# Kernel optimization log

Measured on AMD Instinct MI355X. Metric: run time of the kernel, lower is better.

The kernel has to match this reference:

```python
import jax, jax.numpy as jnp
import numpy as np

B, N, D = 1, 65536, 1024
H = 512
R = 16  # num_regions
C = 2   # num_classes

def _gelu(x):
    return jax.nn.gelu(x, approximate=False)  # torch nn.GELU default is exact erf

def setup_inputs() -> dict:
    key = jax.random.key(0)
    ks = jax.random.split(key, 16)
    s = 0.02
    return {
        "embeddings": jax.random.normal(ks[0], (B, N, D), dtype=jnp.float32),
        # region_encoder: Linear(D,H) + GELU (dropout=0 in eval)
        "W1": jax.random.normal(ks[1], (D, H), dtype=jnp.float32) * s,
        "b1": jnp.zeros((H,), dtype=jnp.float32),
        # region_attention: Linear(H,H//2) -> tanh -> Linear(H//2,1)
        "Wa1": jax.random.normal(ks[2], (H, H // 2), dtype=jnp.float32) * s,
        "ba1": jnp.zeros((H // 2,), dtype=jnp.float32),
        "Wa2": jax.random.normal(ks[3], (H // 2, 1), dtype=jnp.float32) * s,
        "ba2": jnp.zeros((1,), dtype=jnp.float32),
        # slide_encoder: Linear(H,H) + GELU
        "Ws": jax.random.normal(ks[4], (H, H), dtype=jnp.float32) * s,
        "bs": jnp.zeros((H,), dtype=jnp.float32),
        # slide_attention
        "Wsa1": jax.random.normal(ks[5], (H, H // 2), dtype=jnp.float32) * s,
        "bsa1": jnp.zeros((H // 2,), dtype=jnp.float32),
        "Wsa2": jax.random.normal(ks[6], (H // 2, 1), dtype=jnp.float32) * s,
        "bsa2": jnp.zeros((1,), dtype=jnp.float32),
        # classifier: Linear(H,H//2) -> GELU -> Linear(H//2,C)
        "Wc1": jax.random.normal(ks[7], (H, H // 2), dtype=jnp.float32) * s,
        "bc1": jnp.zeros((H // 2,), dtype=jnp.float32),
        "Wc2": jax.random.normal(ks[8], (H // 2, C), dtype=jnp.float32) * s,
        "bc2": jnp.zeros((C,), dtype=jnp.float32),
    }

def reference(embeddings, W1, b1, Wa1, ba1, Wa2, ba2, Ws, bs, Wsa1, bsa1, Wsa2, bsa2, Wc1, bc1, Wc2, bc2):
    b, n, d = embeddings.shape
    m = n // R  # patches per region
    # coords=None path: region_ids[i] = i % R, so region r holds indices r, r+R, ...
    # Equivalent regrouping via reshape+transpose: (B, M, R, D) -> (B, R, M, D)
    x = embeddings.reshape(b, m, R, d).transpose(0, 2, 1, 3)
    # region encoder
    region_emb = _gelu(jnp.einsum('brmd,dh->brmh', x, W1) + b1)  # (B,R,M,H)
    # region attention pooling
    scores = jnp.einsum('brmk,ko->brmo', jnp.tanh(jnp.einsum('brmh,hk->brmk', region_emb, Wa1) + ba1), Wa2) + ba2  # (B,R,M,1)
    attn = jax.nn.softmax(scores, axis=2)
    region_features = jnp.sum(region_emb * attn, axis=2)  # (B,R,H)
    # slide encoder + attention pooling over regions
    slide_emb = _gelu(jnp.einsum('brh,hg->brg', region_features, Ws) + bs)  # (B,R,H)
    sattn = jnp.einsum('brk,ko->bro', jnp.tanh(jnp.einsum('brh,hk->brk', slide_emb, Wsa1) + bsa1), Wsa2) + bsa2  # (B,R,1)
    sweights = jax.nn.softmax(sattn, axis=1)
    slide_rep = jnp.sum(slide_emb * sweights, axis=1)  # (B,H)
    # classifier
    logits = _gelu(slide_rep @ Wc1 + bc1) @ Wc2 + bc2  # (B,C)
    return logits
```

## Files before the change

### kernel.cpp

```cpp
#include <hip/hip_runtime.h>

#define NTOK 65536
#define DIN  1024
#define H    512
#define HH   256
#define NREG 16
#define MPR  4096

__device__ __forceinline__ unsigned short f2bf(float f) {
  unsigned u = __float_as_uint(f);
  u += 0x7fffu + ((u >> 16) & 1u);
  return (unsigned short)(u >> 16);
}
__device__ __forceinline__ float bf2f(unsigned short s) {
  return __uint_as_float(((unsigned)s) << 16);
}
__device__ __forceinline__ float gelu_exact(float x) {
  return 0.5f * x * (1.0f + erff(x * 0.70710678118654752440f));
}

typedef __attribute__((ext_vector_type(8))) short shortx8;
typedef __attribute__((ext_vector_type(4))) float floatx4;

__device__ __forceinline__ void gl_lds16(const void* g, void* l) {
  __builtin_amdgcn_global_load_lds(
      (const __attribute__((address_space(1))) void*)g,
      (__attribute__((address_space(3))) void*)l, 16, 0, 0);
}

__global__ __launch_bounds__(256) void k0_prep(const float* __restrict__ W1,
                                               const float* __restrict__ Wa1,
                                               unsigned short* __restrict__ W1t,
                                               unsigned short* __restrict__ Wa1t) {
  int idx = blockIdx.x * 256 + threadIdx.x;
  if (idx < DIN * H) {
    int n = idx >> 10, k = idx & 1023;
    W1t[idx] = f2bf(W1[k * H + n]);
  } else {
    int i2 = idx - DIN * H;
    int n = i2 >> 9, k = i2 & 511;
    Wa1t[i2] = f2bf(Wa1[k * HH + n]);
  }
}

__global__ __launch_bounds__(256) void k1_gemm1(const float* __restrict__ X,
                                                const unsigned short* __restrict__ W1t,
                                                const float* __restrict__ b1,
                                                unsigned short* __restrict__ Eb) {
  __shared__ __align__(16) short lA[128 * 32];
  __shared__ __align__(16) short lB[128 * 32];
  const int tid = threadIdx.x;
  const int colBase = blockIdx.x * 128;
  const int rowBase = blockIdx.y * 128;
  const int lane = tid & 63;
  const int wave = tid >> 6;
  const int wr = wave >> 1, wc = wave & 1;
  const int l15 = lane & 15, quad = lane >> 4;

  floatx4 acc[4][4] = {};

  for (int kb = 0; kb < DIN; kb += 32) {
    __syncthreads();
#pragma unroll
    for (int s = 0; s < 2; s++) {
      int c = tid + s * 256;
      gl_lds16(W1t + (size_t)(colBase + (c >> 2)) * DIN + kb + (c & 3) * 8, &lB[c * 8]);
    }
#pragma unroll
    for (int s = 0; s < 2; s++) {
      int c = tid + s * 256;
      const floatx4* src =
          (const floatx4*)(X + (size_t)(rowBase + (c >> 2)) * DIN + kb + (c & 3) * 8);
      floatx4 f0 = src[0], f1 = src[1];
      shortx8 h;
      h[0] = (short)f2bf(f0[0]); h[1] = (short)f2bf(f0[1]);
      h[2] = (short)f2bf(f0[2]); h[3] = (short)f2bf(f0[3]);
      h[4] = (short)f2bf(f1[0]); h[5] = (short)f2bf(f1[1]);
      h[6] = (short)f2bf(f1[2]); h[7] = (short)f2bf(f1[3]);
      *(shortx8*)(&lA[c * 8]) = h;
    }
    __syncthreads();
    shortx8 aF[4], bF[4];
#pragma unroll
    for (int i = 0; i < 4; i++)
      aF[i] = *(const shortx8*)(&lA[(wr * 64 + i * 16 + l15) * 32 + quad * 8]);
#pragma unroll
    for (int j = 0; j < 4; j++)
      bF[j] = *(const shortx8*)(&lB[(wc * 64 + j * 16 + l15) * 32 + quad * 8]);
#pragma unroll
    for (int i = 0; i < 4; i++)
#pragma unroll
      for (int j = 0; j < 4; j++)
        acc[i][j] = __builtin_amdgcn_mfma_f32_16x16x32_bf16(aF[i], bF[j], acc[i][j], 0, 0, 0);
  }

  const int row0 = rowBase + wr * 64;
  const int col0 = colBase + wc * 64;
#pragma unroll
  for (int j = 0; j < 4; j++) {
    int col = col0 + j * 16 + l15;
    float bias = b1[col];
#pragma unroll
    for (int i = 0; i < 4; i++) {
      int rb = row0 + i * 16 + quad * 4;
#pragma unroll
      for (int v = 0; v < 4; v++) {
        float x = acc[i][j][v] + bias;
        Eb[(size_t)(rb + v) * H + col] = f2bf(gelu_exact(x));
      }
    }
  }
}

__global__ __launch_bounds__(256) void k2_gemm2(const unsigned short* __restrict__ Eb,
                                                const unsigned short* __restrict__ Wa1t,
                                                const float* __restrict__ ba1,
                                                const float* __restrict__ Wa2,
                                                float* __restrict__ scores) {
  __shared__ __align__(16) short lA[128 * 32];
  __shared__ __align__(16) short lB[128 * 32];
  const int tid = threadIdx.x;
  const int colBase = blockIdx.x * 128;
  const int rowBase = blockIdx.y * 128;
  const int lane = tid & 63;
  const int wave = tid >> 6;
  const int wr = wave >> 1, wc = wave & 1;
  const int l15 = lane & 15, quad = lane >> 4;

  floatx4 acc[4][4] = {};

  for (int kb = 0; kb < H; kb += 32) {
    __syncthreads();
#pragma unroll
    for (int s = 0; s < 2; s++) {
      int c = tid + s * 256;
      gl_lds16(Eb + (size_t)(rowBase + (c >> 2)) * H + kb + (c & 3) * 8, &lA[c * 8]);
      gl_lds16(Wa1t + (size_t)(colBase + (c >> 2)) * H + kb + (c & 3) * 8, &lB[c * 8]);
    }
    __syncthreads();
    shortx8 aF[4], bF[4];
#pragma unroll
    for (int i = 0; i < 4; i++)
      aF[i] = *(const shortx8*)(&lA[(wr * 64 + i * 16 + l15) * 32 + quad * 8]);
#pragma unroll
    for (int j = 0; j < 4; j++)
      bF[j] = *(const shortx8*)(&lB[(wc * 64 + j * 16 + l15) * 32 + quad * 8]);
#pragma unroll
    for (int i = 0; i < 4; i++)
#pragma unroll
      for (int j = 0; j < 4; j++)
        acc[i][j] = __builtin_amdgcn_mfma_f32_16x16x32_bf16(aF[i], bF[j], acc[i][j], 0, 0, 0);
  }

  float p[4][4];
#pragma unroll
  for (int i = 0; i < 4; i++)
#pragma unroll
    for (int v = 0; v < 4; v++) p[i][v] = 0.0f;
#pragma unroll
  for (int j = 0; j < 4; j++) {
    int col = colBase + wc * 64 + j * 16 + l15;
    float bias = ba1[col];
    float wa2 = Wa2[col];
#pragma unroll
    for (int i = 0; i < 4; i++)
#pragma unroll
      for (int v = 0; v < 4; v++)
        p[i][v] += tanhf(acc[i][j][v] + bias) * wa2;
  }
#pragma unroll
  for (int i = 0; i < 4; i++)
#pragma unroll
    for (int v = 0; v < 4; v++) {
      float t = p[i][v];
      t += __shfl_xor(t, 1, 16);
      t += __shfl_xor(t, 2, 16);
      t += __shfl_xor(t, 4, 16);
      t += __shfl_xor(t, 8, 16);
      p[i][v] = t;
    }
  if (l15 == 0) {
    int row0 = rowBase + wr * 64 + quad * 4;
#pragma unroll
    for (int i = 0; i < 4; i++)
#pragma unroll
      for (int v = 0; v < 4; v++)
        atomicAdd(&scores[row0 + i * 16 + v], p[i][v]);
  }
}

__global__ __launch_bounds__(256) void k3a_softmax(const float* __restrict__ scores,
                                                   float* __restrict__ wts) {
  const int r = blockIdx.x, tid = threadIdx.x;
  __shared__ float red[256];
  float m = -1e30f;
  for (int j = tid; j < MPR; j += 256) m = fmaxf(m, scores[r + NREG * j]);
  red[tid] = m;
  __syncthreads();
  for (int s = 128; s > 0; s >>= 1) {
    if (tid < s) red[tid] = fmaxf(red[tid], red[tid + s]);
    __syncthreads();
  }
  float mx = red[0];
  __syncthreads();
  float sum = 0.0f;
  for (int j = tid; j < MPR; j += 256) sum += expf(scores[r + NREG * j] - mx);
  red[tid] = sum;
  __syncthreads();
  for (int s = 128; s > 0; s >>= 1) {
    if (tid < s) red[tid] += red[tid + s];
    __syncthreads();
  }
  float inv = 1.0f / red[0];
  for (int j = tid; j < MPR; j += 256)
    wts[r + NREG * j] = expf(scores[r + NREG * j] - mx) * inv;
}

__global__ __launch_bounds__(256) void k3b_wsum(const unsigned short* __restrict__ Eb,
                                                const float* __restrict__ wts,
                                                float* __restrict__ rf) {
  const int r = blockIdx.y;
  const int mc = blockIdx.x;
  const int tid = threadIdx.x;
  float a0 = 0.0f, a1 = 0.0f;
  for (int j = mc * 128; j < mc * 128 + 128; j++) {
    int n = r + NREG * j;
    float w = wts[n];
    unsigned v = *(const unsigned*)(Eb + (size_t)n * H + tid * 2);
    a0 += w * bf2f((unsigned short)(v & 0xffffu));
    a1 += w * bf2f((unsigned short)(v >> 16));
  }
  atomicAdd(&rf[r * H + tid * 2], a0);
  atomicAdd(&rf[r * H + tid * 2 + 1], a1);
}

__global__ __launch_bounds__(256) void k4a_slide(const float* __restrict__ rf,
                                                 const float* __restrict__ Ws,
                                                 const float* __restrict__ bs,
                                                 float* __restrict__ se) {
  const int r = blockIdx.x, tid = threadIdx.x;
  __shared__ float lrf[H];
  lrf[tid] = rf[r * H + tid];
  lrf[tid + 256] = rf[r * H + tid + 256];
  __syncthreads();
  float a0 = 0.0f, a1 = 0.0f;
  for (int k = 0; k < H; k++) {
    float x = lrf[k];
    a0 += x * Ws[k * H + tid];
    a1 += x * Ws[k * H + tid + 256];
  }
  se[r * H + tid] = gelu_exact(a0 + bs[tid]);
  se[r * H + tid + 256] = gelu_exact(a1 + bs[tid + 256]);
}

__global__ __launch_bounds__(256) void k4b_sscore(const float* __restrict__ se,
                                                  const float* __restrict__ Wsa1,
                                                  const float* __restrict__ bsa1,
                                                  const float* __restrict__ Wsa2,
                                                  const float* __restrict__ bsa2,
                                                  float* __restrict__ ss) {
  const int r = blockIdx.x, tid = threadIdx.x;
  __shared__ float lse[H];
  __shared__ float red[256];
  lse[tid] = se[r * H + tid];
  lse[tid + 256] = se[r * H + tid + 256];
  __syncthreads();
  float a = 0.0f;
  for (int k = 0; k < H; k++) a += lse[k] * Wsa1[k * HH + tid];
  red[tid] = tanhf(a + bsa1[tid]) * Wsa2[tid];
  __syncthreads();
  for (int s = 128; s > 0; s >>= 1) {
    if (tid < s) red[tid] += red[tid + s];
    __syncthreads();
  }
  if (tid == 0) ss[r] = red[0] + bsa2[0];
}

__global__ __launch_bounds__(256) void k4c_final(const float* __restrict__ se,
                                                 const float* __restrict__ ss,
                                                 const float* __restrict__ Wc1,
                                                 const float* __restrict__ bc1,
                                                 const float* __restrict__ Wc2,
                                                 const float* __restrict__ bc2,
                                                 float* __restrict__ out) {
  const int tid = threadIdx.x;
  __shared__ float srep[H];
  __shared__ float r0[256], r1[256];
  float mx = -1e30f;
  for (int i = 0; i < NREG; i++) mx = fmaxf(mx, ss[i]);
  float wv[NREG];
  float den = 0.0f;
  for (int i = 0; i < NREG; i++) { wv[i] = expf(ss[i] - mx); den += wv[i]; }
  float inv = 1.0f / den;
  float s0 = 0.0f, s1 = 0.0f;
  for (int i = 0; i < NREG; i++) {
    float w = wv[i] * inv;
    s0 += w * se[i * H + tid];
    s1 += w * se[i * H + tid + 256];
  }
  srep[tid] = s0;
  srep[tid + 256] = s1;
  __syncthreads();
  float a = 0.0f;
  for (int k = 0; k < H; k++) a += srep[k] * Wc1[k * HH + tid];
  float g = gelu_exact(a + bc1[tid]);
  r0[tid] = g * Wc2[tid * 2];
  r1[tid] = g * Wc2[tid * 2 + 1];
  __syncthreads();
  for (int s = 128; s > 0; s >>= 1) {
    if (tid < s) { r0[tid] += r0[tid + s]; r1[tid] += r1[tid + s]; }
    __syncthreads();
  }
  if (tid == 0) {
    out[0] = r0[0] + bc2[0];
    out[1] = r1[0] + bc2[1];
  }
}

extern "C" void kernel_launch(void* const* d_in, const int* in_sizes, int n_in,
                              void* d_out, int out_size, void* d_ws, size_t ws_size,
                              hipStream_t stream) {
  const float* X    = (const float*)d_in[0];
  const float* W1   = (const float*)d_in[1];
  const float* b1   = (const float*)d_in[2];
  const float* Wa1  = (const float*)d_in[3];
  const float* ba1  = (const float*)d_in[4];
  const float* Wa2  = (const float*)d_in[5];
  const float* Ws   = (const float*)d_in[7];
  const float* bs   = (const float*)d_in[8];
  const float* Wsa1 = (const float*)d_in[9];
  const float* bsa1 = (const float*)d_in[10];
  const float* Wsa2 = (const float*)d_in[11];
  const float* bsa2 = (const float*)d_in[12];
  const float* Wc1  = (const float*)d_in[13];
  const float* bc1  = (const float*)d_in[14];
  const float* Wc2  = (const float*)d_in[15];
  const float* bc2  = (const float*)d_in[16];
  float* out = (float*)d_out;

  char* ws = (char*)d_ws;
  constexpr size_t OFF_W1T  = 0;
  constexpr size_t OFF_WA1T = OFF_W1T + (size_t)H * DIN * 2;
  constexpr size_t OFF_EB   = OFF_WA1T + (size_t)HH * H * 2;
  constexpr size_t OFF_SC   = OFF_EB + (size_t)NTOK * H * 2;
  constexpr size_t OFF_RF   = OFF_SC + (size_t)NTOK * 4;
  constexpr size_t OFF_WT   = OFF_RF + (size_t)NREG * H * 4;
  constexpr size_t OFF_SE   = OFF_WT + (size_t)NTOK * 4;
  constexpr size_t OFF_SS   = OFF_SE + (size_t)NREG * H * 4;

  unsigned short* W1t  = (unsigned short*)(ws + OFF_W1T);
  unsigned short* Wa1t = (unsigned short*)(ws + OFF_WA1T);
  unsigned short* Eb   = (unsigned short*)(ws + OFF_EB);
  float* scores = (float*)(ws + OFF_SC);
  float* rf     = (float*)(ws + OFF_RF);
  float* wts    = (float*)(ws + OFF_WT);
  float* se     = (float*)(ws + OFF_SE);
  float* ssb    = (float*)(ws + OFF_SS);

  hipMemsetAsync(scores, 0, (size_t)NTOK * 4 + (size_t)NREG * H * 4, stream);

  k0_prep<<<(DIN * H + HH * H) / 256, 256, 0, stream>>>(W1, Wa1, W1t, Wa1t);
  k1_gemm1<<<dim3(4, 512), 256, 0, stream>>>(X, W1t, b1, Eb);
  k2_gemm2<<<dim3(2, 512), 256, 0, stream>>>(Eb, Wa1t, ba1, Wa2, scores);
  k3a_softmax<<<NREG, 256, 0, stream>>>(scores, wts);
  k3b_wsum<<<dim3(32, NREG), 256, 0, stream>>>(Eb, wts, rf);
  k4a_slide<<<NREG, 256, 0, stream>>>(rf, Ws, bs, se);
  k4b_sscore<<<NREG, 256, 0, stream>>>(se, Wsa1, bsa1, Wsa2, bsa2, ssb);
  k4c_final<<<1, 256, 0, stream>>>(se, ssb, Wc1, bc1, Wc2, bc2, out);
}
```

Before: 653.0 us.

## Pre-convert X to bf16 and swizzle LDS tiles in both GEMMs

Adds a separate kernel that converts the fp32 embeddings to bf16 once. GEMM1 can then load its A tile straight from global memory into LDS with direct loads instead of converting in registers each time. Both GEMMs get an XOR swizzle on the k-group layout in LDS to reduce bank conflicts on fragment reads. The trade-off is an extra full pass over X and a large bf16 workspace buffer.

```diff
diff --git a/kernel.cpp b/kernel.cpp
--- a/kernel.cpp
+++ b/kernel.cpp
@@ -26,6 +26,19 @@
   __builtin_amdgcn_global_load_lds(
       (const __attribute__((address_space(1))) void*)g,
       (__attribute__((address_space(3))) void*)l, 16, 0, 0);
+}
+
+__global__ __launch_bounds__(256) void kc_convert(const float* __restrict__ X,
+                                                  unsigned short* __restrict__ Xb) {
+  size_t i = ((size_t)blockIdx.x * 256 + threadIdx.x) * 8;
+  const floatx4* src = (const floatx4*)(X + i);
+  floatx4 f0 = src[0], f1 = src[1];
+  shortx8 h;
+  h[0] = (short)f2bf(f0[0]); h[1] = (short)f2bf(f0[1]);
+  h[2] = (short)f2bf(f0[2]); h[3] = (short)f2bf(f0[3]);
+  h[4] = (short)f2bf(f1[0]); h[5] = (short)f2bf(f1[1]);
+  h[6] = (short)f2bf(f1[2]); h[7] = (short)f2bf(f1[3]);
+  *(shortx8*)(Xb + i) = h;
 }
 
 __global__ __launch_bounds__(256) void k0_prep(const float* __restrict__ W1,
@@ -43,7 +56,8 @@
   }
 }
 
-__global__ __launch_bounds__(256) void k1_gemm1(const float* __restrict__ X,
+
+__global__ __launch_bounds__(256) void k1_gemm1(const unsigned short* __restrict__ Xb,
                                                 const unsigned short* __restrict__ W1t,
                                                 const float* __restrict__ b1,
                                                 unsigned short* __restrict__ Eb) {
@@ -56,6 +70,7 @@
   const int wave = tid >> 6;
   const int wr = wave >> 1, wc = wave & 1;
   const int l15 = lane & 15, quad = lane >> 4;
+  const int sw = (l15 >> 1) & 3;
 
   floatx4 acc[4][4] = {};
 
@@ -64,29 +79,19 @@
 #pragma unroll
     for (int s = 0; s < 2; s++) {
       int c = tid + s * 256;
-      gl_lds16(W1t + (size_t)(colBase + (c >> 2)) * DIN + kb + (c & 3) * 8, &lB[c * 8]);
+      int row = c >> 2;
+      int k16g = (c & 3) ^ ((c >> 3) & 3);
+      gl_lds16(Xb + (size_t)(rowBase + row) * DIN + kb + k16g * 8, &lA[c * 8]);
+      gl_lds16(W1t + (size_t)(colBase + row) * DIN + kb + k16g * 8, &lB[c * 8]);
     }
-#pragma unroll
-    for (int s = 0; s < 2; s++) {
-      int c = tid + s * 256;
-      const floatx4* src =
-          (const floatx4*)(X + (size_t)(rowBase + (c >> 2)) * DIN + kb + (c & 3) * 8);
-      floatx4 f0 = src[0], f1 = src[1];
-      shortx8 h;
-      h[0] = (short)f2bf(f0[0]); h[1] = (short)f2bf(f0[1]);
-      h[2] = (short)f2bf(f0[2]); h[3] = (short)f2bf(f0[3]);
-      h[4] = (short)f2bf(f1[0]); h[5] = (short)f2bf(f1[1]);
-      h[6] = (short)f2bf(f1[2]); h[7] = (short)f2bf(f1[3]);
-      *(shortx8*)(&lA[c * 8]) = h;
-    }
     __syncthreads();
     shortx8 aF[4], bF[4];
 #pragma unroll
     for (int i = 0; i < 4; i++)
-      aF[i] = *(const shortx8*)(&lA[(wr * 64 + i * 16 + l15) * 32 + quad * 8]);
+      aF[i] = *(const shortx8*)(&lA[(wr * 64 + i * 16 + l15) * 32 + (quad ^ sw) * 8]);
 #pragma unroll
     for (int j = 0; j < 4; j++)
-      bF[j] = *(const shortx8*)(&lB[(wc * 64 + j * 16 + l15) * 32 + quad * 8]);
+      bF[j] = *(const shortx8*)(&lB[(wc * 64 + j * 16 + l15) * 32 + (quad ^ sw) * 8]);
 #pragma unroll
     for (int i = 0; i < 4; i++)
 #pragma unroll
@@ -126,6 +131,7 @@
   const int wave = tid >> 6;
   const int wr = wave >> 1, wc = wave & 1;
   const int l15 = lane & 15, quad = lane >> 4;
+  const int sw = (l15 >> 1) & 3;
 
   floatx4 acc[4][4] = {};
 
@@ -134,17 +140,19 @@
 #pragma unroll
     for (int s = 0; s < 2; s++) {
       int c = tid + s * 256;
-      gl_lds16(Eb + (size_t)(rowBase + (c >> 2)) * H + kb + (c & 3) * 8, &lA[c * 8]);
-      gl_lds16(Wa1t + (size_t)(colBase + (c >> 2)) * H + kb + (c & 3) * 8, &lB[c * 8]);
+      int row = c >> 2;
+      int k16g = (c & 3) ^ ((c >> 3) & 3);
+      gl_lds16(Eb + (size_t)(rowBase + row) * H + kb + k16g * 8, &lA[c * 8]);
+      gl_lds16(Wa1t + (size_t)(colBase + row) * H + kb + k16g * 8, &lB[c * 8]);
     }
     __syncthreads();
     shortx8 aF[4], bF[4];
 #pragma unroll
     for (int i = 0; i < 4; i++)
-      aF[i] = *(const shortx8*)(&lA[(wr * 64 + i * 16 + l15) * 32 + quad * 8]);
+      aF[i] = *(const shortx8*)(&lA[(wr * 64 + i * 16 + l15) * 32 + (quad ^ sw) * 8]);
 #pragma unroll
     for (int j = 0; j < 4; j++)
-      bF[j] = *(const shortx8*)(&lB[(wc * 64 + j * 16 + l15) * 32 + quad * 8]);
+      bF[j] = *(const shortx8*)(&lB[(wc * 64 + j * 16 + l15) * 32 + (quad ^ sw) * 8]);
 #pragma unroll
     for (int i = 0; i < 4; i++)
 #pragma unroll
@@ -347,6 +355,7 @@
   constexpr size_t OFF_WT   = OFF_RF + (size_t)NREG * H * 4;
   constexpr size_t OFF_SE   = OFF_WT + (size_t)NTOK * 4;
   constexpr size_t OFF_SS   = OFF_SE + (size_t)NREG * H * 4;
+  constexpr size_t OFF_XB   = OFF_SS + 256;
 
   unsigned short* W1t  = (unsigned short*)(ws + OFF_W1T);
   unsigned short* Wa1t = (unsigned short*)(ws + OFF_WA1T);
@@ -356,11 +365,13 @@
   float* wts    = (float*)(ws + OFF_WT);
   float* se     = (float*)(ws + OFF_SE);
   float* ssb    = (float*)(ws + OFF_SS);
+  unsigned short* Xb = (unsigned short*)(ws + OFF_XB);
 
   hipMemsetAsync(scores, 0, (size_t)NTOK * 4 + (size_t)NREG * H * 4, stream);
 
+  kc_convert<<<(NTOK * (size_t)DIN / 8 + 255) / 256, 256, 0, stream>>>(X, Xb);
   k0_prep<<<(DIN * H + HH * H) / 256, 256, 0, stream>>>(W1, Wa1, W1t, Wa1t);
-  k1_gemm1<<<dim3(4, 512), 256, 0, stream>>>(X, W1t, b1, Eb);
+  k1_gemm1<<<dim3(4, 512), 256, 0, stream>>>(Xb, W1t, b1, Eb);
   k2_gemm2<<<dim3(2, 512), 256, 0, stream>>>(Eb, Wa1t, ba1, Wa2, scores);
   k3a_softmax<<<NREG, 256, 0, stream>>>(scores, wts);
   k3b_wsum<<<dim3(32, NREG), 256, 0, stream>>>(Eb, wts, rf);
```

Result: slower. 670.0 us (+2.6%).
